# Kernel optimization log

Measured on AMD Instinct MI355X. Metric: run time of the kernel, lower is better.

Reference implementation:

```python
import jax, jax.numpy as jnp
import numpy as np

NEG_CLAMP = -100.0  # torch F.binary_cross_entropy clamps log terms at -100


def _ccl_labels(fg):
    """4-connectivity connected-component labeling of a [H,W] bool mask.
    Labels are assigned in raster-scan first-encounter order, matching
    scipy.ndimage.label with the default structure. Background = 0.
    Implemented as min-index label propagation to a fixed point: each
    component ends up tagged with the min flat index of its pixels (its
    first raster-scan pixel), then roots are ranked by cumsum to get 1..num.
    """
    H, W = fg.shape
    INF = H * W  # sentinel larger than any flat index
    idx = jnp.arange(INF, dtype=jnp.int32).reshape(H, W)
    init = jnp.where(fg, idx, INF)

    def step(x):
        up = jnp.concatenate([x[1:], jnp.full((1, W), INF, x.dtype)], axis=0)
        down = jnp.concatenate([jnp.full((1, W), INF, x.dtype), x[:-1]], axis=0)
        left = jnp.concatenate([x[:, 1:], jnp.full((H, 1), INF, x.dtype)], axis=1)
        right = jnp.concatenate([jnp.full((H, 1), INF, x.dtype), x[:, :-1]], axis=1)
        m = jnp.minimum(jnp.minimum(up, down), jnp.minimum(left, right))
        return jnp.where(fg, jnp.minimum(x, m), INF)

    def cond(carry):
        return carry[1]

    def body(carry):
        x, _ = carry
        nx = step(x)
        return nx, jnp.any(nx != x)

    x, _ = jax.lax.while_loop(cond, body, (init, jnp.array(True)))

    flat = x.reshape(-1)
    fgf = fg.reshape(-1)
    # a pixel is the root of its component iff its propagated tag == its own index
    is_root = fgf & (flat == jnp.arange(INF, dtype=jnp.int32))
    rank = jnp.cumsum(is_root.astype(jnp.int32))  # rank[r] = scipy label of root r
    labels = jnp.where(fgf, rank[jnp.clip(flat, 0, INF - 1)], 0)
    return labels.reshape(H, W)


def _target_map(fg):
    """Replicates: labels == labels.flatten()[1:].argmax() + 1 (faithful to source,
    including its quirky use of argmax position as the selected label value)."""
    labels = _ccl_labels(fg)
    lf = labels.reshape(-1)
    v = jnp.argmax(lf[1:]) + 1  # first occurrence of max, like numpy argmax
    return (labels == v).astype(jnp.float32)


def setup_inputs() -> dict:
    key = jax.random.key(0)
    pred = jax.random.uniform(key, (32, 1, 512, 512), dtype=jnp.float32)
    return {"pred": pred}


def reference(pred):
    fg = pred[:, 0] >= 0.5  # [N,H,W] bool
    target = jax.vmap(_target_map)(fg)[:, None]  # [N,1,H,W] float
    logp = jnp.maximum(jnp.log(pred), NEG_CLAMP)
    log1mp = jnp.maximum(jnp.log1p(-pred), NEG_CLAMP)
    return -jnp.mean(target * logp + (1.0 - target) * log1mp)
```

## Files before the change

kernel.cpp:

```cpp
#include <hip/hip_runtime.h>
#include <math.h>

#define IMG_W 512
#define IMG_H 512
#define HW (IMG_W * IMG_H)
#define LOGHW 18
#define NIMG 32
#define NTOT (NIMG * HW)
#define TILE 64
#define TPI 64
#define NTILE (NIMG * TPI)
#define CPI 64
#define NSCHUNK (NIMG * CPI)
#define EDGE_N (NTILE * 64)
#define NPAIR (NIMG * 112)

__device__ __forceinline__ void uf_unite(int* L, int a, int b) {
    while (true) {
        int p = ((volatile int*)L)[a];
        while (p != a) { a = p; p = ((volatile int*)L)[a]; }
        p = ((volatile int*)L)[b];
        while (p != b) { b = p; p = ((volatile int*)L)[b]; }
        if (a == b) return;
        if (a < b) { int t = a; a = b; b = t; }
        int old = atomicMin(&L[a], b);
        if (old == a) return;
        a = old;
    }
}

__global__ __launch_bounds__(1024) void k_local(const float* __restrict__ pred,
                                                int* __restrict__ L,
                                                float* __restrict__ partials,
                                                int* __restrict__ edges,
                                                unsigned int* __restrict__ counter) {
    __shared__ int lab[TILE * TILE];
    __shared__ unsigned long long msk[TILE];
    __shared__ float wsum[16];
    int tile = blockIdx.x;
    int img = tile >> 6;
    int t = tile & (TPI - 1);
    int ty = t >> 3, tx = t & 7;
    int baseLocal = (ty * TILE) * IMG_W + tx * TILE;
    const float* pi = pred + ((size_t)img << LOGHW);
    int* Li = L + ((size_t)img << LOGHW);
    int tid = threadIdx.x;
    int lane = tid & 63, wave = tid >> 6;

    float pv[4];
#pragma unroll
    for (int j = 0; j < 4; j++) {
        int row = wave + j * 16;
        pv[j] = pi[baseLocal + row * IMG_W + lane];
    }
    float acc = 0.0f;
    unsigned long long maskle = (~0ULL) >> (63 - lane);
#pragma unroll
    for (int j = 0; j < 4; j++) {
        int row = wave + j * 16;
        float p = pv[j];
        acc += fmaxf(__logf(1.0f - p), -100.0f);
        bool fg = (p >= 0.5f);
        unsigned long long bal = __ballot(fg);
        if (lane == 0) msk[row] = bal;
        unsigned long long starts = bal & ~(bal << 1);
        if ((starts >> lane) & 1ULL)
            lab[row * TILE + lane] = row * TILE + lane;
    }
    __syncthreads();
#pragma unroll
    for (int j = 0; j < 4; j++) {
        int row = wave + j * 16;
        if (row == 0) continue;
        unsigned long long mc = msk[row], mu = msk[row - 1];
        unsigned long long c = mc & mu;
        unsigned long long cs = c & ~(c << 1);
        if ((cs >> lane) & 1ULL) {
            unsigned long long stc = mc & ~(mc << 1);
            unsigned long long stu = mu & ~(mu << 1);
            int a = row * TILE + (63 - __builtin_clzll(stc & maskle));
            int b = (row - 1) * TILE + (63 - __builtin_clzll(stu & maskle));
            uf_unite(lab, a, b);
        }
    }
    __syncthreads();
#pragma unroll
    for (int j = 0; j < 4; j++) {
        int row = wave + j * 16;
        unsigned long long m = msk[row];
        unsigned long long st = m & ~(m << 1);
        if ((st >> lane) & 1ULL) {
            int i = row * TILE + lane;
            int x = i, p = lab[x];
            while (p != x) {
                int g = lab[p];
                lab[x] = g;
                x = g;
                p = lab[x];
            }
            lab[i] = x;
        }
    }
    __syncthreads();
    {
        int i4 = tid * 4;
        int row = i4 >> 6, lx = i4 & 63;
        unsigned long long m = msk[row];
        unsigned long long st = m & ~(m << 1);
        int4 o;
        int* op = (int*)&o;
#pragma unroll
        for (int k = 0; k < 4; k++) {
            int l = lx + k;
            if (!((m >> l) & 1ULL)) op[k] = -1;
            else {
                unsigned long long pre = st & ((~0ULL) >> (63 - l));
                int s = row * TILE + (63 - __builtin_clzll(pre));
                int r = lab[s];
                op[k] = baseLocal + (r >> 6) * IMG_W + (r & 63);
            }
        }
        *(int4*)(Li + baseLocal + row * IMG_W + lx) = o;
    }
    if (tid < 256) {
        int e = tid >> 6;
        int q = tid & 63;
        int val = -1;
        if (e == 0) {
            unsigned long long m = msk[0];
            if ((m >> q) & 1ULL) {
                unsigned long long st = m & ~(m << 1);
                int s = 63 - __builtin_clzll(st & ((~0ULL) >> (63 - q)));
                int r = lab[s];
                val = baseLocal + (r >> 6) * IMG_W + (r & 63);
            }
        } else if (e == 1) {
            unsigned long long m = msk[63];
            if ((m >> q) & 1ULL) {
                unsigned long long st = m & ~(m << 1);
                int s = 63 * TILE + (63 - __builtin_clzll(st & ((~0ULL) >> (63 - q))));
                int r = lab[s];
                val = baseLocal + (r >> 6) * IMG_W + (r & 63);
            }
        } else if (e == 2) {
            unsigned long long m = msk[q];
            if (m & 1ULL) {
                int r = lab[q * TILE];
                val = baseLocal + (r >> 6) * IMG_W + (r & 63);
            }
        } else {
            unsigned long long m = msk[q];
            if ((m >> 63) & 1ULL) {
                unsigned long long st = m & ~(m << 1);
                int s = q * TILE + (63 - __builtin_clzll(st));
                int r = lab[s];
                val = baseLocal + (r >> 6) * IMG_W + (r & 63);
            }
        }
        edges[e * EDGE_N + tile * 64 + q] = val;
    }
#pragma unroll
    for (int off = 32; off > 0; off >>= 1)
        acc += __shfl_down(acc, off, 64);
    if (lane == 0) wsum[wave] = acc;
    __syncthreads();
    if (tid == 0) {
        float s = 0.0f;
#pragma unroll
        for (int w = 0; w < 16; w++) s += wsum[w];
        partials[blockIdx.x] = s;
    }
    if (blockIdx.x == 0 && tid == 0) *counter = 0u;
}

__global__ __launch_bounds__(256) void k_border(const int* __restrict__ edges,
                                                int* __restrict__ L) {
    int gid = blockIdx.x * blockDim.x + threadIdx.x;
    int pair = gid >> 6;
    int lane = gid & 63;
    int a, b, img;
    if (pair < NIMG * 56) {
        img = pair / 56;
        int w = pair - img * 56;
        int ty = w / 7, tx = w - ty * 7;
        int tl = img * TPI + ty * 8 + tx;
        a = edges[3 * EDGE_N + tl * 64 + lane];
        b = edges[2 * EDGE_N + (tl + 1) * 64 + lane];
    } else {
        int p2 = pair - NIMG * 56;
        img = p2 / 56;
        int w = p2 - img * 56;
        int ty = w >> 3, tx = w & 7;
        int tu = img * TPI + ty * 8 + tx;
        a = edges[1 * EDGE_N + tu * 64 + lane];
        b = edges[0 * EDGE_N + (tu + 8) * 64 + lane];
    }
    bool c = (a >= 0) && (b >= 0);
    unsigned long long cb = __ballot(c);
    unsigned long long cs = cb & ~(cb << 1);
    if ((cs >> lane) & 1ULL)
        uf_unite(L + ((size_t)img << LOGHW), a, b);
}

__global__ __launch_bounds__(256) void k_stats(const int* __restrict__ L,
                                               int* __restrict__ cntArr,
                                               int* __restrict__ maxArr,
                                               int* __restrict__ minArr) {
    __shared__ int s1[256], s2[256], s3[256];
    int chunk = blockIdx.x;
    int img = chunk >> 6;
    int baseL = (chunk & 63) * 4096;
    const int* Li = L + ((size_t)img << LOGHW);
    int t = threadIdx.x;
    int cnt = 0, mx = -1, mn = HW;
#pragma unroll
    for (int j = 0; j < 4; j++) {
        int off = baseL + (t + j * 256) * 4;
        int4 l4 = *(const int4*)(Li + off);
        const int* lp = (const int*)&l4;
#pragma unroll
        for (int k = 0; k < 4; k++) {
            int local = off + k;
            int p = lp[k];
            bool root = (p == local);
            cnt += root ? 1 : 0;
            if (root && local > mx) mx = local;
            if (p >= 0 && local >= 1 && local < mn) mn = local;
        }
    }
    s1[t] = cnt; s2[t] = mx; s3[t] = mn;
    __syncthreads();
    for (int s = 128; s > 0; s >>= 1) {
        if (t < s) {
            s1[t] += s1[t + s];
            s2[t] = max(s2[t], s2[t + s]);
            s3[t] = min(s3[t], s3[t + s]);
        }
        __syncthreads();
    }
    if (t == 0) { cntArr[chunk] = s1[0]; maxArr[chunk] = s2[0]; minArr[chunk] = s3[0]; }
}

__global__ __launch_bounds__(256) void k_tail(const int* __restrict__ cntArr,
                                              const int* __restrict__ maxArr,
                                              const int* __restrict__ minArr,
                                              const int* __restrict__ L,
                                              const float* __restrict__ pred,
                                              const float* __restrict__ partials,
                                              float* __restrict__ corr,
                                              unsigned int* __restrict__ counter,
                                              float* __restrict__ out) {
    __shared__ int sc[256], sm[256], sn[256];
    __shared__ int sel_chunk, sel_base, result;
    __shared__ float sf[256];
    __shared__ double sd[256];
    __shared__ unsigned int oldc;
    int img = blockIdx.x, t = threadIdx.x;
    const int* Li = L + ((size_t)img << LOGHW);
    int cnt = (t < CPI) ? cntArr[img * CPI + t] : 0;
    sc[t] = cnt;
    sm[t] = (t < CPI) ? maxArr[img * CPI + t] : -1;
    sn[t] = (t < CPI) ? minArr[img * CPI + t] : HW;
    if (t == 0) result = -2;
    __syncthreads();
    for (int off = 1; off < 256; off <<= 1) {
        int v2 = (t >= off) ? sc[t - off] : 0;
        __syncthreads();
        sc[t] += v2;
        __syncthreads();
    }
    int num = sc[255];
    int inc = sc[t], exc = inc - cnt;
    for (int s = 128; s > 0; s >>= 1) {
        if (t < s) { sm[t] = max(sm[t], sm[t + s]); sn[t] = min(sn[t], sn[t + s]); }
        __syncthreads();
    }
    int last_root = sm[0], minFg = sn[0];
    int v;
    if (last_root >= 1) v = last_root;
    else if (last_root == 0) v = (minFg < HW) ? minFg : 1;
    else v = 1;
    if (v >= 1 && v <= num) {
        if (exc < v && v <= inc) { sel_chunk = t; sel_base = exc; }
        __syncthreads();
        int c = sel_chunk, base = sel_base;
        int baseL = c * 4096;
        int f[16];
        int sum = 0;
#pragma unroll
        for (int j = 0; j < 4; j++) {
            int off = baseL + t * 16 + j * 4;
            int4 l4 = *(const int4*)(Li + off);
            const int* lp = (const int*)&l4;
#pragma unroll
            for (int k = 0; k < 4; k++) {
                f[j * 4 + k] = (lp[k] == off + k) ? 1 : 0;
                sum += f[j * 4 + k];
            }
        }
        __syncthreads();
        sc[t] = sum;
        __syncthreads();
        for (int off = 1; off < 256; off <<= 1) {
            int v2 = (t >= off) ? sc[t - off] : 0;
            __syncthreads();
            sc[t] += v2;
            __syncthreads();
        }
        int exc2 = sc[t] - sum;
        int need = v - base;
        if (exc2 < need && need <= sc[t]) {
            int run = exc2;
#pragma unroll
            for (int k = 0; k < 16; k++) {
                run += f[k];
                if (run == need) { result = baseL + t * 16 + k; break; }
            }
        }
        __syncthreads();
    } else {
        __syncthreads();
    }
    int rvv = result;
    float blocksum = 0.0f;
    if (rvv >= 0) {
        const float* pi = pred + ((size_t)img << LOGHW);
        float acc = 0.0f;
        for (int it = 0; it < HW / 1024; it++) {
            int off = it * 1024 + t * 4;
            float4 p4 = *(const float4*)(pi + off);
            int4 l4 = *(const int4*)(Li + off);
            const float* pp = (const float*)&p4;
            const int* lp = (const int*)&l4;
#pragma unroll
            for (int k = 0; k < 4; k++) {
                int p = lp[k];
                if (p < 0) continue;
                int x = p, q = Li[x];
                while (q != x) { x = q; q = Li[x]; }
                if (x == rvv) {
                    float pr = pp[k];
                    acc += fmaxf(__logf(pr), -100.0f)
                         - fmaxf(__logf(1.0f - pr), -100.0f);
                }
            }
        }
        sf[t] = acc;
        __syncthreads();
        for (int s = 128; s > 0; s >>= 1) {
            if (t < s) sf[t] += sf[t + s];
            __syncthreads();
        }
        blocksum = sf[0];
    }
    if (t == 0) {
        __hip_atomic_store(&corr[img], blocksum, __ATOMIC_RELAXED,
                           __HIP_MEMORY_SCOPE_AGENT);
        oldc = __hip_atomic_fetch_add(counter, 1u, __ATOMIC_ACQ_REL,
                                      __HIP_MEMORY_SCOPE_AGENT);
    }
    __syncthreads();
    if (oldc != NIMG - 1) return;
    double acc = 0.0;
#pragma unroll
    for (int j = 0; j < 8; j++) acc += (double)partials[t + j * 256];
    if (t < NIMG)
        acc += (double)__hip_atomic_load(&corr[t], __ATOMIC_ACQUIRE,
                                         __HIP_MEMORY_SCOPE_AGENT);
    sd[t] = acc;
    __syncthreads();
    for (int s = 128; s > 0; s >>= 1) {
        if (t < s) sd[t] += sd[t + s];
        __syncthreads();
    }
    if (t == 0) out[0] = (float)(-sd[0] / (double)NTOT);
}

extern "C" void kernel_launch(void* const* d_in, const int* in_sizes, int n_in,
                              void* d_out, int out_size, void* d_ws, size_t ws_size,
                              hipStream_t stream) {
    const float* pred = (const float*)d_in[0];
    float* out = (float*)d_out;

    char* ws = (char*)d_ws;
    int* L = (int*)ws;
    int* edges = (int*)(ws + (size_t)NTOT * 4);
    int* cntArr = edges + 4 * EDGE_N;
    int* maxArr = cntArr + NSCHUNK;
    int* minArr = maxArr + NSCHUNK;
    float* partials = (float*)(minArr + NSCHUNK);
    float* corr = partials + NTILE;
    unsigned int* counter = (unsigned int*)(corr + NIMG);

    k_local<<<dim3(NTILE), dim3(1024), 0, stream>>>(pred, L, partials, edges, counter);
    k_border<<<dim3(NPAIR * 64 / 256), dim3(256), 0, stream>>>(edges, L);
    k_stats<<<dim3(NSCHUNK), dim3(256), 0, stream>>>(L, cntArr, maxArr, minArr);
    k_tail<<<dim3(NIMG), dim3(256), 0, stream>>>(cntArr, maxArr, minArr, L, pred,
                                                 partials, corr, counter, out);
}
```

Measured before the change: 124.3 us.

## Split streaming pass into bitmask kernel and separate tile CCL kernel

Adds a lightweight streaming kernel that reads the prediction with full-row coalesced loads, accumulates the log(1-p) partial sums and writes a packed per-row foreground bitmask. The tile CCL kernel then reads only these 64-bit masks instead of float pixels, so the heavy 1024-thread shared-memory kernel no longer waits on global loads. The first union in each row is simplified to a find plus atomicMin, falling back to the full unite only on conflict. This costs one extra launch and a small mask buffer round trip.

Result: slower. 129.3 us (+4.1%).

```diff
diff --git a/kernel.cpp b/kernel.cpp
--- a/kernel.cpp
+++ b/kernel.cpp
@@ -29,42 +29,61 @@
     }
 }
 
-__global__ __launch_bounds__(1024) void k_local(const float* __restrict__ pred,
-                                                int* __restrict__ L,
+__global__ __launch_bounds__(256) void k_stream(const float* __restrict__ pred,
+                                                unsigned long long* __restrict__ maskbuf,
                                                 float* __restrict__ partials,
-                                                int* __restrict__ edges,
                                                 unsigned int* __restrict__ counter) {
+    __shared__ float wsum[4];
+    int b = blockIdx.x;
+    int img = b >> 6;
+    int y0 = (b & 63) * 8;
+    int tid = threadIdx.x;
+    int lane = tid & 63, wave = tid >> 6;
+    const float* pi = pred + ((size_t)img << LOGHW);
+    float acc = 0.0f;
+#pragma unroll
+    for (int i = 0; i < 16; i++) {
+        int row = y0 + 2 * wave + (i >> 3);
+        int seg = i & 7;
+        float p = pi[row * IMG_W + seg * 64 + lane];
+        acc += fmaxf(__logf(1.0f - p), -100.0f);
+        unsigned long long bal = __ballot(p >= 0.5f);
+        if (lane == 0) maskbuf[((size_t)(img << 9) + row) * 8 + seg] = bal;
+    }
+#pragma unroll
+    for (int off = 32; off > 0; off >>= 1)
+        acc += __shfl_down(acc, off, 64);
+    if (lane == 0) wsum[wave] = acc;
+    __syncthreads();
+    if (tid == 0)
+        partials[b] = wsum[0] + wsum[1] + wsum[2] + wsum[3];
+    if (b == 0 && tid == 0) *counter = 0u;
+}
+
+__global__ __launch_bounds__(1024) void k_ccl(const unsigned long long* __restrict__ maskbuf,
+                                              int* __restrict__ L,
+                                              int* __restrict__ edges) {
     __shared__ int lab[TILE * TILE];
     __shared__ unsigned long long msk[TILE];
-    __shared__ float wsum[16];
     int tile = blockIdx.x;
     int img = tile >> 6;
     int t = tile & (TPI - 1);
     int ty = t >> 3, tx = t & 7;
     int baseLocal = (ty * TILE) * IMG_W + tx * TILE;
-    const float* pi = pred + ((size_t)img << LOGHW);
     int* Li = L + ((size_t)img << LOGHW);
     int tid = threadIdx.x;
     int lane = tid & 63, wave = tid >> 6;
 
-    float pv[4];
+    if (tid < 64)
+        msk[tid] = maskbuf[((size_t)(img << 9) + ty * 64 + tid) * 8 + tx];
+    __syncthreads();
+    unsigned long long maskle = (~0ULL) >> (63 - lane);
 #pragma unroll
     for (int j = 0; j < 4; j++) {
         int row = wave + j * 16;
-        pv[j] = pi[baseLocal + row * IMG_W + lane];
-    }
-    float acc = 0.0f;
-    unsigned long long maskle = (~0ULL) >> (63 - lane);
-#pragma unroll
-    for (int j = 0; j < 4; j++) {
-        int row = wave + j * 16;
-        float p = pv[j];
-        acc += fmaxf(__logf(1.0f - p), -100.0f);
-        bool fg = (p >= 0.5f);
-        unsigned long long bal = __ballot(fg);
-        if (lane == 0) msk[row] = bal;
-        unsigned long long starts = bal & ~(bal << 1);
-        if ((starts >> lane) & 1ULL)
+        unsigned long long m = msk[row];
+        unsigned long long st = m & ~(m << 1);
+        if ((st >> lane) & 1ULL)
             lab[row * TILE + lane] = row * TILE + lane;
     }
     __syncthreads();
@@ -80,7 +99,10 @@
             unsigned long long stu = mu & ~(mu << 1);
             int a = row * TILE + (63 - __builtin_clzll(stc & maskle));
             int b = (row - 1) * TILE + (63 - __builtin_clzll(stu & maskle));
-            uf_unite(lab, a, b);
+            int x = b, p = ((volatile int*)lab)[x];
+            while (p != x) { x = p; p = ((volatile int*)lab)[x]; }
+            int old = atomicMin(&lab[a], x);
+            if (old != a && old != x) uf_unite(lab, old, x);
         }
     }
     __syncthreads();
@@ -159,18 +181,6 @@
         }
         edges[e * EDGE_N + tile * 64 + q] = val;
     }
-#pragma unroll
-    for (int off = 32; off > 0; off >>= 1)
-        acc += __shfl_down(acc, off, 64);
-    if (lane == 0) wsum[wave] = acc;
-    __syncthreads();
-    if (tid == 0) {
-        float s = 0.0f;
-#pragma unroll
-        for (int w = 0; w < 16; w++) s += wsum[w];
-        partials[blockIdx.x] = s;
-    }
-    if (blockIdx.x == 0 && tid == 0) *counter = 0u;
 }
 
 __global__ __launch_bounds__(256) void k_border(const int* __restrict__ edges,
@@ -385,14 +395,17 @@
     char* ws = (char*)d_ws;
     int* L = (int*)ws;
     int* edges = (int*)(ws + (size_t)NTOT * 4);
-    int* cntArr = edges + 4 * EDGE_N;
+    unsigned long long* maskbuf =
+        (unsigned long long*)(edges + 4 * EDGE_N);
+    int* cntArr = (int*)(maskbuf + NIMG * 512 * 8);
     int* maxArr = cntArr + NSCHUNK;
     int* minArr = maxArr + NSCHUNK;
     float* partials = (float*)(minArr + NSCHUNK);
     float* corr = partials + NTILE;
     unsigned int* counter = (unsigned int*)(corr + NIMG);
 
-    k_local<<<dim3(NTILE), dim3(1024), 0, stream>>>(pred, L, partials, edges, counter);
+    k_stream<<<dim3(NTILE), dim3(256), 0, stream>>>(pred, maskbuf, partials, counter);
+    k_ccl<<<dim3(NTILE), dim3(1024), 0, stream>>>(maskbuf, L, edges);
     k_border<<<dim3(NPAIR * 64 / 256), dim3(256), 0, stream>>>(edges, L);
     k_stats<<<dim3(NSCHUNK), dim3(256), 0, stream>>>(L, cntArr, maxArr, minArr);
     k_tail<<<dim3(NIMG), dim3(256), 0, stream>>>(cntArr, maxArr, minArr, L, pred,
```
